# Performance work log

Measured on AMD Instinct MI355X. Metric: run time of the kernel, lower is better.

## Reference

```python
import jax, jax.numpy as jnp
import numpy as np

jax.config.update("jax_enable_x64", True)  # faithful int64 hash arithmetic

N2_SIZES = [6619, 6637, 6653, 6659, 6661, 6673, 6679, 6689]
N3_SIZES = [65521, 65537, 65539, 65543, 65551, 65557, 65563, 65579]
SLOT_DIM = 80  # 1280 / (2 orders * 8 heads)
NUM_HEADS = 8
BATCH, SEQ = 8, 4096
VOCAB = 50257


def setup_inputs() -> dict:
    key = jax.random.key(0)
    ks = jax.random.split(key, 2 + 16)
    inp = {
        "canonical_ids": jax.random.randint(ks[0], (BATCH, SEQ), 0, VOCAB, dtype=jnp.int64),
        "hash_seeds": jax.random.randint(ks[1], (3, NUM_HEADS), 1, 2**31 - 1, dtype=jnp.int64),
    }
    i = 2
    for n, sizes in ((2, N2_SIZES), (3, N3_SIZES)):
        for h, sz in enumerate(sizes):
            inp[f"w_n{n}_h{h}"] = 0.02 * jax.random.normal(ks[i], (sz, SLOT_DIM), dtype=jnp.float32)
            i += 1
    return inp


def _ngrams(ids, n):
    # suffix n-grams per position, left-padded with 0: [B, S, n]
    padded = jnp.pad(ids, ((0, 0), (n - 1, 0)))
    S = ids.shape[1]
    return jnp.stack([padded[:, i:i + S] for i in range(n)], axis=-1)


def reference(canonical_ids, hash_seeds,
              w_n2_h0, w_n2_h1, w_n2_h2, w_n2_h3, w_n2_h4, w_n2_h5, w_n2_h6, w_n2_h7,
              w_n3_h0, w_n3_h1, w_n3_h2, w_n3_h3, w_n3_h4, w_n3_h5, w_n3_h6, w_n3_h7):
    tables = {
        2: [w_n2_h0, w_n2_h1, w_n2_h2, w_n2_h3, w_n2_h4, w_n2_h5, w_n2_h6, w_n2_h7],
        3: [w_n3_h0, w_n3_h1, w_n3_h2, w_n3_h3, w_n3_h4, w_n3_h5, w_n3_h6, w_n3_h7],
    }
    sizes = {2: N2_SIZES, 3: N3_SIZES}
    outs = []
    for n in (2, 3):
        ng = _ngrams(canonical_ids, n)                              # [B, S, n] int64
        seeds = hash_seeds[:n].T                                    # [H, n]
        terms = ng[:, :, None, :] * seeds[None, None, :, :]         # [B, S, H, n]
        h = terms[..., 0]
        for i in range(1, n):
            h = h ^ terms[..., i]                                   # [B, S, H]
        for k in range(NUM_HEADS):
            idx = h[:, :, k] % sizes[n][k]                          # [B, S]
            outs.append(tables[n][k][idx])                          # [B, S, SLOT_DIM]
    return jnp.concatenate(outs, axis=-1)                           # [B, S, 1280]
```

## Files before the change

### kernel.cpp

```cpp
#include <hip/hip_runtime.h>

typedef unsigned long long ull;

__global__ __launch_bounds__(256, 4)
void engram_kernel(const int* __restrict__ ids,
                   const int* __restrict__ seeds,
                   const float* __restrict__ t0,  const float* __restrict__ t1,
                   const float* __restrict__ t2,  const float* __restrict__ t3,
                   const float* __restrict__ t4,  const float* __restrict__ t5,
                   const float* __restrict__ t6,  const float* __restrict__ t7,
                   const float* __restrict__ t8,  const float* __restrict__ t9,
                   const float* __restrict__ t10, const float* __restrict__ t11,
                   const float* __restrict__ t12, const float* __restrict__ t13,
                   const float* __restrict__ t14, const float* __restrict__ t15,
                   float* __restrict__ out)
{
    __shared__ const float* tab[16];
    __shared__ int szs[16];
    if (threadIdx.x == 0) {
        tab[0]=t0;  tab[1]=t1;  tab[2]=t2;  tab[3]=t3;
        tab[4]=t4;  tab[5]=t5;  tab[6]=t6;  tab[7]=t7;
        tab[8]=t8;  tab[9]=t9;  tab[10]=t10; tab[11]=t11;
        tab[12]=t12; tab[13]=t13; tab[14]=t14; tab[15]=t15;
        szs[0]=6619;  szs[1]=6637;  szs[2]=6653;  szs[3]=6659;
        szs[4]=6661;  szs[5]=6673;  szs[6]=6679;  szs[7]=6689;
        szs[8]=65521; szs[9]=65537; szs[10]=65539; szs[11]=65543;
        szs[12]=65551; szs[13]=65557; szs[14]=65563; szs[15]=65579;
    }
    __syncthreads();

    const int wave = threadIdx.x >> 6;
    const int lane = threadIdx.x & 63;
    const int pos  = blockIdx.x * 4 + wave;
    const int b = pos >> 12;
    const int s = pos & 4095;

    const int* row = ids + (b << 12);
    const int id0  = row[s];
    const int idm1 = (s >= 1) ? row[s - 1] : 0;
    const int idm2 = (s >= 2) ? row[s - 2] : 0;

    const int slot = lane & 15;
    const int head = slot & 7;
    const ull sa = (ull)(unsigned)seeds[head];
    const ull sb = (ull)(unsigned)seeds[8 + head];
    ull h;
    if (slot < 8) {
        h = ((ull)(unsigned)idm1 * sa) ^ ((ull)(unsigned)id0 * sb);
    } else {
        const ull sc = (ull)(unsigned)seeds[16 + head];
        h = ((ull)(unsigned)idm2 * sa) ^ ((ull)(unsigned)idm1 * sb)
            ^ ((ull)(unsigned)id0 * sc);
    }
    const unsigned sz  = (unsigned)szs[slot];
    const unsigned idx = (unsigned)(h % (ull)sz);

    float4* dst = (float4*)out + (size_t)pos * 320;
    #pragma unroll
    for (int j = 0; j < 5; ++j) {
        const int g  = lane + (j << 6);
        const int gs = g / 20;
        const int off = g - gs * 20;
        const unsigned ridx = (unsigned)__shfl((int)idx, gs, 64);
        const float4* src = (const float4*)tab[gs] + (size_t)ridx * 20 + off;
        dst[g] = *src;
    }
}

extern "C" void kernel_launch(void* const* d_in, const int* in_sizes, int n_in,
                              void* d_out, int out_size, void* d_ws, size_t ws_size,
                              hipStream_t stream) {
    const int* ids   = (const int*)d_in[0];
    const int* seeds = (const int*)d_in[1];
    const float* t[16];
    for (int i = 0; i < 16; ++i) t[i] = (const float*)d_in[2 + i];

    engram_kernel<<<dim3(8192), dim3(256), 0, stream>>>(
        ids, seeds,
        t[0], t[1], t[2], t[3], t[4], t[5], t[6], t[7],
        t[8], t[9], t[10], t[11], t[12], t[13], t[14], t[15],
        (float*)d_out);
}
```

Before: 320.0 us.

## Split hash computation and row gather into two kernels with nontemporal stores

Moves the n-gram hashing and modulo into a separate kernel that writes 16 row indices per position to workspace. A second kernel then launches one 320-thread block per position, where each thread loads one float4 from its table and writes it with a nontemporal store, with no shuffles. This is meant to take the 64-bit modulo and shuffle work off the bandwidth-bound gather path and avoid output cache pollution. In exchange it adds a second launch, an index round-trip through global memory, and many small blocks.

```diff
diff --git a/kernel.cpp b/kernel.cpp
--- a/kernel.cpp
+++ b/kernel.cpp
@@ -1,46 +1,28 @@
 #include <hip/hip_runtime.h>
 
 typedef unsigned long long ull;
+typedef float f4 __attribute__((ext_vector_type(4)));
 
-__global__ __launch_bounds__(256, 4)
-void engram_kernel(const int* __restrict__ ids,
-                   const int* __restrict__ seeds,
-                   const float* __restrict__ t0,  const float* __restrict__ t1,
-                   const float* __restrict__ t2,  const float* __restrict__ t3,
-                   const float* __restrict__ t4,  const float* __restrict__ t5,
-                   const float* __restrict__ t6,  const float* __restrict__ t7,
-                   const float* __restrict__ t8,  const float* __restrict__ t9,
-                   const float* __restrict__ t10, const float* __restrict__ t11,
-                   const float* __restrict__ t12, const float* __restrict__ t13,
-                   const float* __restrict__ t14, const float* __restrict__ t15,
-                   float* __restrict__ out)
+__constant__ unsigned kSizes[16] = {
+    6619u, 6637u, 6653u, 6659u, 6661u, 6673u, 6679u, 6689u,
+    65521u, 65537u, 65539u, 65543u, 65551u, 65557u, 65563u, 65579u
+};
+
+__global__ __launch_bounds__(256)
+void engram_idx_kernel(const int* __restrict__ ids,
+                       const int* __restrict__ seeds,
+                       int* __restrict__ idx_out)
 {
-    __shared__ const float* tab[16];
-    __shared__ int szs[16];
-    if (threadIdx.x == 0) {
-        tab[0]=t0;  tab[1]=t1;  tab[2]=t2;  tab[3]=t3;
-        tab[4]=t4;  tab[5]=t5;  tab[6]=t6;  tab[7]=t7;
-        tab[8]=t8;  tab[9]=t9;  tab[10]=t10; tab[11]=t11;
-        tab[12]=t12; tab[13]=t13; tab[14]=t14; tab[15]=t15;
-        szs[0]=6619;  szs[1]=6637;  szs[2]=6653;  szs[3]=6659;
-        szs[4]=6661;  szs[5]=6673;  szs[6]=6679;  szs[7]=6689;
-        szs[8]=65521; szs[9]=65537; szs[10]=65539; szs[11]=65543;
-        szs[12]=65551; szs[13]=65557; szs[14]=65563; szs[15]=65579;
-    }
-    __syncthreads();
-
-    const int wave = threadIdx.x >> 6;
-    const int lane = threadIdx.x & 63;
-    const int pos  = blockIdx.x * 4 + wave;
+    const int tid  = blockIdx.x * 256 + threadIdx.x;
+    const int pos  = tid >> 4;
+    const int slot = tid & 15;
     const int b = pos >> 12;
     const int s = pos & 4095;
 
     const int* row = ids + (b << 12);
     const int id0  = row[s];
     const int idm1 = (s >= 1) ? row[s - 1] : 0;
-    const int idm2 = (s >= 2) ? row[s - 2] : 0;
 
-    const int slot = lane & 15;
     const int head = slot & 7;
     const ull sa = (ull)(unsigned)seeds[head];
     const ull sb = (ull)(unsigned)seeds[8 + head];
@@ -48,23 +30,44 @@
     if (slot < 8) {
         h = ((ull)(unsigned)idm1 * sa) ^ ((ull)(unsigned)id0 * sb);
     } else {
+        const int idm2 = (s >= 2) ? row[s - 2] : 0;
         const ull sc = (ull)(unsigned)seeds[16 + head];
         h = ((ull)(unsigned)idm2 * sa) ^ ((ull)(unsigned)idm1 * sb)
             ^ ((ull)(unsigned)id0 * sc);
     }
-    const unsigned sz  = (unsigned)szs[slot];
-    const unsigned idx = (unsigned)(h % (ull)sz);
+    idx_out[tid] = (int)(h % (ull)kSizes[slot]);
+}
 
-    float4* dst = (float4*)out + (size_t)pos * 320;
-    #pragma unroll
-    for (int j = 0; j < 5; ++j) {
-        const int g  = lane + (j << 6);
-        const int gs = g / 20;
-        const int off = g - gs * 20;
-        const unsigned ridx = (unsigned)__shfl((int)idx, gs, 64);
-        const float4* src = (const float4*)tab[gs] + (size_t)ridx * 20 + off;
-        dst[g] = *src;
+__global__ __launch_bounds__(320)
+void engram_gather_kernel(const int* __restrict__ idx_in,
+                          const float* __restrict__ t0,  const float* __restrict__ t1,
+                          const float* __restrict__ t2,  const float* __restrict__ t3,
+                          const float* __restrict__ t4,  const float* __restrict__ t5,
+                          const float* __restrict__ t6,  const float* __restrict__ t7,
+                          const float* __restrict__ t8,  const float* __restrict__ t9,
+                          const float* __restrict__ t10, const float* __restrict__ t11,
+                          const float* __restrict__ t12, const float* __restrict__ t13,
+                          const float* __restrict__ t14, const float* __restrict__ t15,
+                          f4* __restrict__ out)
+{
+    __shared__ const f4* tab[16];
+    if (threadIdx.x == 0) {
+        tab[0]=(const f4*)t0;   tab[1]=(const f4*)t1;   tab[2]=(const f4*)t2;   tab[3]=(const f4*)t3;
+        tab[4]=(const f4*)t4;   tab[5]=(const f4*)t5;   tab[6]=(const f4*)t6;   tab[7]=(const f4*)t7;
+        tab[8]=(const f4*)t8;   tab[9]=(const f4*)t9;   tab[10]=(const f4*)t10; tab[11]=(const f4*)t11;
+        tab[12]=(const f4*)t12; tab[13]=(const f4*)t13; tab[14]=(const f4*)t14; tab[15]=(const f4*)t15;
     }
+    __syncthreads();
+
+    const int pos  = blockIdx.x;
+    const int tx   = threadIdx.x;
+    const int slot = tx / 20;
+    const int off  = tx - slot * 20;
+
+    const int ridx = idx_in[pos * 16 + slot];
+    const f4  v    = tab[slot][ridx * 20 + off];
+
+    __builtin_nontemporal_store(v, out + (size_t)pos * 320 + tx);
 }
 
 extern "C" void kernel_launch(void* const* d_in, const int* in_sizes, int n_in,
@@ -75,9 +78,13 @@
     const float* t[16];
     for (int i = 0; i < 16; ++i) t[i] = (const float*)d_in[2 + i];
 
-    engram_kernel<<<dim3(8192), dim3(256), 0, stream>>>(
-        ids, seeds,
+    int* idx_buf = (int*)d_ws;
+
+    engram_idx_kernel<<<dim3(2048), dim3(256), 0, stream>>>(ids, seeds, idx_buf);
+
+    engram_gather_kernel<<<dim3(32768), dim3(320), 0, stream>>>(
+        idx_buf,
         t[0], t[1], t[2], t[3], t[4], t[5], t[6], t[7],
         t[8], t[9], t[10], t[11], t[12], t[13], t[14], t[15],
-        (float*)d_out);
+        (f4*)d_out);
 }
```

Result: slower. 329.6 us (+3.0%).
